# Kernel tuning notes

Measured on AMD Instinct MI355X. Metric: run time of the kernel, lower is better.

Reference implementation:

```python
import jax, jax.numpy as jnp
import numpy as np

B, P, EPG = 1000, 100, 1200  # graphs, nodes/graph, edges/graph
IN, HID, OUT, K = 16, 64, 5, 3


def setup_inputs() -> dict:
    key = jax.random.key(0)
    ks = jax.random.split(key, 12)
    offs = jnp.repeat(jnp.arange(B, dtype=jnp.int32) * P, EPG)
    src = jax.random.randint(ks[0], (B * EPG,), 0, P, dtype=jnp.int32) + offs
    dst = jax.random.randint(ks[1], (B * EPG,), 0, P, dtype=jnp.int32) + offs
    graph_ids = jnp.repeat(jnp.arange(B, dtype=jnp.int32), P)
    feat = jax.random.normal(ks[2], (B * P, IN), dtype=jnp.float32)

    def lin(k1, fan_in, fan_out):
        s = 1.0 / np.sqrt(fan_in)
        return jax.random.uniform(k1, (fan_in, fan_out), jnp.float32, -s, s)

    return {
        'feat': feat, 'src': src, 'dst': dst, 'graph_ids': graph_ids,
        'n_graphs': B,
        'W1': lin(ks[3], K * IN, HID), 'b1': jnp.zeros((HID,), jnp.float32),
        'W2': lin(ks[4], K * HID, HID), 'b2': jnp.zeros((HID,), jnp.float32),
        'W3': lin(ks[5], K * HID, HID), 'b3': jnp.zeros((HID,), jnp.float32),
        'Wfc': lin(ks[6], HID, OUT), 'bfc': jnp.zeros((OUT,), jnp.float32),
    }


def _cheb_conv(x, src, dst, d_invsqrt, W, b, k):
    # DGL ChebConv with lambda_max=2 -> re_norm=1, scaled Laplacian = -D^-1/2 A D^-1/2
    n = x.shape[0]

    def Ax(h):
        msg = (h * d_invsqrt)[src]                      # gather from source nodes
        agg = jax.ops.segment_sum(msg, dst, num_segments=n)
        return agg * d_invsqrt

    Xs = [x]
    if k > 1:
        Xs.append(-Ax(Xs[0]))                           # X1 = L_hat X0
        for _ in range(2, k):
            Xs.append(-2.0 * Ax(Xs[-1]) - Xs[-2])       # X_i = 2 L_hat X_{i-1} - X_{i-2}
    Xt = jnp.concatenate(Xs, axis=1)                    # [n, k*f]
    return Xt @ W + b


def reference(feat, src, dst, graph_ids, n_graphs, W1, b1, W2, b2, W3, b3, Wfc, bfc):
    n = feat.shape[0]
    deg = jax.ops.segment_sum(jnp.ones((src.shape[0],), feat.dtype), dst, num_segments=n)
    d_invsqrt = jnp.where(deg < 1.0, 1.0, deg) ** -0.5
    d_invsqrt = d_invsqrt[:, None]

    h = jax.nn.relu(_cheb_conv(feat, src, dst, d_invsqrt, W1, b1, K))
    h = jax.nn.relu(_cheb_conv(h, src, dst, d_invsqrt, W2, b2, K))
    h = jax.nn.relu(_cheb_conv(h, src, dst, d_invsqrt, W3, b3, K))

    # dgl.mean_nodes: per-graph mean pooling
    counts = jax.ops.segment_sum(jnp.ones((n,), h.dtype), graph_ids, num_segments=n_graphs)
    hg = jax.ops.segment_sum(h, graph_ids, num_segments=n_graphs) / counts[:, None]
    return hg @ Wfc + bfc
```

## Files before the change

kernel.cpp:

```cpp
#include <hip/hip_runtime.h>

#define NGRAPH 1000
#define P      100
#define EPG    1200
#define INF    16
#define HID    64
#define NOUT   5

#define ASTR   88
#define T2OFF  72
#define SLOTA  64
#define SLOTB  80
#define NPAD   112


typedef short short8 __attribute__((ext_vector_type(8)));
typedef float f32x4  __attribute__((ext_vector_type(4)));

__device__ __forceinline__ void bsplit(float x, short& h, short& l) {
    unsigned u = __float_as_uint(x);
    h = (short)(u >> 16);
    float hf = __uint_as_float(u & 0xffff0000u);
    l = (short)(__float_as_uint(x - hf) >> 16);
}

__device__ __forceinline__ void prop_x1(
    float* __restrict__ A, int soff, int dslot,
    const unsigned char* __restrict__ csr_src,
    const int* __restrict__ csr_off,
    const float* __restrict__ dinv, int tid)
{
    const int q4 = (tid & 1) * 4;
    const int n  = tid >> 1;
    if (n < P) {
        const int kb = csr_off[n], ke = csr_off[n + 1];
        float ax = 0.f, ay = 0.f, az = 0.f, aw = 0.f;
        for (int k = kb; k < ke; k++) {
            int s = csr_src[k];
            const float4 x = *(const float4*)&A[s * ASTR + soff + q4];
            ax += x.x; ay += x.y; az += x.z; aw += x.w;
        }
        float dn = dinv[n];
        float m = -dn * dn;
        float4 o; o.x = m * ax; o.y = m * ay; o.z = m * az; o.w = m * aw;
        *(float4*)&A[n * ASTR + dslot + q4] = o;
    }
}

__device__ __forceinline__ void prop_dual(
    float* __restrict__ A, int t1c, int t1n, int ycur, int ynext, bool pre,
    const unsigned char* __restrict__ csr_src,
    const int* __restrict__ csr_off,
    const float* __restrict__ dinv, int tid)
{
    const int q4 = (tid & 1) * 4;
    const int n  = tid >> 1;
    if (n < P) {
        const int kb = csr_off[n], ke = csr_off[n + 1];
        float4 a2 = make_float4(0.f, 0.f, 0.f, 0.f);
        float4 a1 = make_float4(0.f, 0.f, 0.f, 0.f);
        if (pre) {
            for (int k = kb; k < ke; k++) {
                int s = csr_src[k];
                const float* rp = &A[s * ASTR + q4];
                const float4 x2 = *(const float4*)&rp[t1c];
                const float4 x1 = *(const float4*)&rp[ynext];
                a2.x += x2.x; a2.y += x2.y; a2.z += x2.z; a2.w += x2.w;
                a1.x += x1.x; a1.y += x1.y; a1.z += x1.z; a1.w += x1.w;
            }
        } else {
            for (int k = kb; k < ke; k++) {
                int s = csr_src[k];
                const float4 x2 = *(const float4*)&A[s * ASTR + t1c + q4];
                a2.x += x2.x; a2.y += x2.y; a2.z += x2.z; a2.w += x2.w;
            }
        }
        float dn = dinv[n];
        float d2 = dn * dn;
        const float4 y0 = *(const float4*)&A[n * ASTR + ycur + q4];
        float4 o2;
        float m2 = -2.f * d2;
        o2.x = m2 * a2.x - y0.x; o2.y = m2 * a2.y - y0.y;
        o2.z = m2 * a2.z - y0.z; o2.w = m2 * a2.w - y0.w;
        *(float4*)&A[n * ASTR + T2OFF + q4] = o2;
        if (pre) {
            float m1 = -d2;
            float4 o1;
            o1.x = m1 * a1.x; o1.y = m1 * a1.y;
            o1.z = m1 * a1.z; o1.w = m1 * a1.w;
            *(float4*)&A[n * ASTR + t1n + q4] = o1;
        }
    }
}

template <int F, int FINAL>
__device__ __forceinline__ void cheb_layer(
    float* __restrict__ A,
    const unsigned char* __restrict__ csr_src,
    const int* __restrict__ csr_off,
    const float* __restrict__ dinv,
    const float* __restrict__ W, const float* __restrict__ bias,
    int tid)
{
    const int lane = tid & 63;
    const int wv   = tid >> 6;
    const int n16  = lane & 15;
    const int q    = lane >> 4;
    const int ncol = (wv << 4) + n16;
    const float qsc = (q < 3) ? 1.f : 0.f;

    f32x4 acc[7];
#pragma unroll
    for (int t = 0; t < 7; t++) { acc[t][0]=0.f; acc[t][1]=0.f; acc[t][2]=0.f; acc[t][3]=0.f; }

    prop_x1(A, 0, SLOTA, csr_src, csr_off, dinv, tid);
    __syncthreads();

    int t1c = SLOTA, t1n = SLOTB;
    for (int cb = 0; cb < F; cb += 8) {
        const bool pre = (cb + 8 < F);
        prop_dual(A, t1c, t1n, cb, cb + 8, pre, csr_src, csr_off, dinv, tid);
        __syncthreads();

        const int wrow = (q == 0) ? cb : (q == 1) ? (F + cb)
                       : (q == 2) ? (2 * F + cb) : cb;
        short8 bhi, blo;
#pragma unroll
        for (int j = 0; j < 8; j++) {
            float b = W[(wrow + j) * HID + ncol] * qsc;
            short h, l; bsplit(b, h, l);
            bhi[j] = h; blo[j] = l;
        }
        const int aoff = (q == 0) ? cb : (q == 1) ? t1c
                       : (q == 2) ? T2OFF : cb;
#pragma unroll
        for (int t = 0; t < 7; t++) {
            const float* xp = &A[(t * 16 + n16) * ASTR + aoff];
            const float4 v0 = *(const float4*)xp;
            const float4 v1 = *(const float4*)(xp + 4);
            short8 ahi, alo; short h, l;
            bsplit(v0.x * qsc, h, l); ahi[0] = h; alo[0] = l;
            bsplit(v0.y * qsc, h, l); ahi[1] = h; alo[1] = l;
            bsplit(v0.z * qsc, h, l); ahi[2] = h; alo[2] = l;
            bsplit(v0.w * qsc, h, l); ahi[3] = h; alo[3] = l;
            bsplit(v1.x * qsc, h, l); ahi[4] = h; alo[4] = l;
            bsplit(v1.y * qsc, h, l); ahi[5] = h; alo[5] = l;
            bsplit(v1.z * qsc, h, l); ahi[6] = h; alo[6] = l;
            bsplit(v1.w * qsc, h, l); ahi[7] = h; alo[7] = l;
            acc[t] = __builtin_amdgcn_mfma_f32_16x16x32_bf16(ahi, bhi, acc[t], 0, 0, 0);
            acc[t] = __builtin_amdgcn_mfma_f32_16x16x32_bf16(ahi, blo, acc[t], 0, 0, 0);
            acc[t] = __builtin_amdgcn_mfma_f32_16x16x32_bf16(alo, bhi, acc[t], 0, 0, 0);
        }
        __syncthreads();
        int tt = t1c; t1c = t1n; t1n = tt;
    }

    const float bcol = bias[ncol];
    const int rbase = q * 4;
#pragma unroll
    for (int t = 0; t < 7; t++) {
#pragma unroll
        for (int r = 0; r < 4; r++) {
            int row = t * 16 + rbase + r;
            if (row < P) {
                float dn = dinv[row];
                float v = acc[t][r];
                float o;
                if (FINAL) o = fmaxf(v * (1.0f / dn) + bcol, 0.f);
                else       o = fmaxf(v + bcol * dn, 0.f);
                A[row * ASTR + ncol] = o;
            }
        }
    }
    __syncthreads();
}

__global__ __launch_bounds__(256, 4) void gnn_kernel(
    const float* __restrict__ feat,
    const int* __restrict__ src, const int* __restrict__ dst,
    const float* __restrict__ W1, const float* __restrict__ b1,
    const float* __restrict__ W2, const float* __restrict__ b2,
    const float* __restrict__ W3, const float* __restrict__ b3,
    const float* __restrict__ Wfc, const float* __restrict__ bfc,
    float* __restrict__ out)
{
    __shared__ __align__(16) float A[NPAD * ASTR];
    __shared__ unsigned char csr_src[EPG];

    const int g = blockIdx.x;
    const int tid = threadIdx.x;
    const int base = g * P;
    const int* srcg = src + g * EPG;
    const int* dstg = dst + g * EPG;

    int*   deg     = (int*)&A[P * ASTR];
    int*   cur     = (int*)&A[P * ASTR + 100];
    int*   csr_off = (int*)&A[P * ASTR + 200];
    float* dinv    = &A[P * ASTR + 304];
    float* psum    = &A[P * ASTR + 404];

    for (int i = tid; i < P; i += 256) deg[i] = 0;
    __syncthreads();
    for (int e = tid; e < EPG; e += 256) {
        int d = dstg[e] - base;
        atomicAdd(&deg[d], 1);
    }
    __syncthreads();

    for (int i = tid; i < P; i += 256) {
        int dg = deg[i] > 1 ? deg[i] : 1;
        dinv[i] = rsqrtf((float)dg);
    }
    if (tid == 0) {
        int run = 0;
        csr_off[0] = 0;
        for (int i = 0; i < P; i++) { run += deg[i]; csr_off[i + 1] = run; }
    }
    __syncthreads();

    for (int i = tid; i < P * INF / 4; i += 256) {
        int n = i >> 2, fq = (i & 3) * 4;
        float4 v = *(const float4*)&feat[(size_t)base * INF + i * 4];
        float dn = dinv[n];
        v.x *= dn; v.y *= dn; v.z *= dn; v.w *= dn;
        *(float4*)&A[n * ASTR + fq] = v;
    }
    for (int i = tid; i < P; i += 256) cur[i] = csr_off[i];
    __syncthreads();
    for (int e = tid; e < EPG; e += 256) {
        int s = srcg[e] - base;
        int d = dstg[e] - base;
        int pos = atomicAdd(&cur[d], 1);
        csr_src[pos] = (unsigned char)s;
    }
    __syncthreads();

    cheb_layer<INF, 0>(A, csr_src, csr_off, dinv, W1, b1, tid);
    cheb_layer<HID, 0>(A, csr_src, csr_off, dinv, W2, b2, tid);
    cheb_layer<HID, 1>(A, csr_src, csr_off, dinv, W3, b3, tid);

    {
        const int lane = tid & 63, w = tid >> 6;
        float s = 0.f;
        for (int n = w; n < P; n += 4) s += A[n * ASTR + lane];
        psum[w * 64 + lane] = s;
    }
    __syncthreads();
    if (tid < HID) {
        float hg = (psum[tid] + psum[64 + tid] + psum[128 + tid] + psum[192 + tid]) * (1.0f / P);
        psum[256 + tid] = hg;
    }
    __syncthreads();
    if (tid < NOUT) {
        float o = bfc[tid];
        for (int c = 0; c < HID; c++) o += psum[256 + c] * Wfc[c * NOUT + tid];
        out[g * NOUT + tid] = o;
    }
}

extern "C" void kernel_launch(void* const* d_in, const int* in_sizes, int n_in,
                              void* d_out, int out_size, void* d_ws, size_t ws_size,
                              hipStream_t stream)
{
    const float* feat = (const float*)d_in[0];
    const int*   src  = (const int*)d_in[1];
    const int*   dst  = (const int*)d_in[2];
    const float* W1  = (const float*)d_in[5];
    const float* b1  = (const float*)d_in[6];
    const float* W2  = (const float*)d_in[7];
    const float* b2  = (const float*)d_in[8];
    const float* W3  = (const float*)d_in[9];
    const float* b3  = (const float*)d_in[10];
    const float* Wfc = (const float*)d_in[11];
    const float* bfc = (const float*)d_in[12];
    float* out = (float*)d_out;

    gnn_kernel<<<NGRAPH, 256, 0, stream>>>(feat, src, dst,
                                           W1, b1, W2, b2, W3, b3, Wfc, bfc, out);
}
```

Baseline: 191.4 us.

## Pre-split weights into bf16 hi/lo and store activations in packed hi/lo form

```diff
diff --git a/kernel.cpp b/kernel.cpp
--- a/kernel.cpp
+++ b/kernel.cpp
@@ -15,13 +15,51 @@
 
 
 typedef short short8 __attribute__((ext_vector_type(8)));
+typedef int   int4v  __attribute__((ext_vector_type(4)));
 typedef float f32x4  __attribute__((ext_vector_type(4)));
-
-__device__ __forceinline__ void bsplit(float x, short& h, short& l) {
+union HL { int4v i; short8 s; };
+
+__device__ __forceinline__ float funp(float f) {
+    unsigned p = __float_as_uint(f);
+    return __uint_as_float(p & 0xffff0000u) + __uint_as_float(p << 16);
+}
+__device__ __forceinline__ float fpk(float x) {
     unsigned u = __float_as_uint(x);
-    h = (short)(u >> 16);
-    float hf = __uint_as_float(u & 0xffff0000u);
-    l = (short)(__float_as_uint(x - hf) >> 16);
+    unsigned hb = u & 0xffff0000u;
+    float lo = x - __uint_as_float(hb);
+    return __uint_as_float(hb | (__float_as_uint(lo) >> 16));
+}
+
+__global__ __launch_bounds__(256) void wprep(
+    const float* __restrict__ W1, const float* __restrict__ W2,
+    const float* __restrict__ W3, short* __restrict__ wt)
+{
+    const int i0 = blockIdx.x * blockDim.x + threadIdx.x;
+    const int stride = gridDim.x * blockDim.x;
+    for (int e = i0; e < HID * 56; e += stride) {
+        int c = e / 56, r = e % 56;
+        float v = (r < 48) ? W1[r * HID + c] : 0.f;
+        unsigned u = __float_as_uint(v);
+        unsigned hb = u & 0xffff0000u;
+        float lo = v - __uint_as_float(hb);
+        wt[e]        = (short)(hb >> 16);
+        wt[3584 + e] = (short)(__float_as_uint(lo) >> 16);
+    }
+    for (int e = i0; e < HID * 200; e += stride) {
+        int c = e / 200, r = e % 200;
+        float v2 = (r < 192) ? W2[r * HID + c] : 0.f;
+        float v3 = (r < 192) ? W3[r * HID + c] : 0.f;
+        unsigned u2 = __float_as_uint(v2);
+        unsigned h2 = u2 & 0xffff0000u;
+        float l2 = v2 - __uint_as_float(h2);
+        wt[7168 + e]  = (short)(h2 >> 16);
+        wt[19968 + e] = (short)(__float_as_uint(l2) >> 16);
+        unsigned u3 = __float_as_uint(v3);
+        unsigned h3 = u3 & 0xffff0000u;
+        float l3 = v3 - __uint_as_float(h3);
+        wt[32768 + e] = (short)(h3 >> 16);
+        wt[45568 + e] = (short)(__float_as_uint(l3) >> 16);
+    }
 }
 
 __device__ __forceinline__ void prop_x1(
@@ -38,11 +76,12 @@
         for (int k = kb; k < ke; k++) {
             int s = csr_src[k];
             const float4 x = *(const float4*)&A[s * ASTR + soff + q4];
-            ax += x.x; ay += x.y; az += x.z; aw += x.w;
+            ax += funp(x.x); ay += funp(x.y); az += funp(x.z); aw += funp(x.w);
         }
         float dn = dinv[n];
         float m = -dn * dn;
-        float4 o; o.x = m * ax; o.y = m * ay; o.z = m * az; o.w = m * aw;
+        float4 o;
+        o.x = fpk(m * ax); o.y = fpk(m * ay); o.z = fpk(m * az); o.w = fpk(m * aw);
         *(float4*)&A[n * ASTR + dslot + q4] = o;
     }
 }
@@ -65,29 +104,32 @@
                 const float* rp = &A[s * ASTR + q4];
                 const float4 x2 = *(const float4*)&rp[t1c];
                 const float4 x1 = *(const float4*)&rp[ynext];
-                a2.x += x2.x; a2.y += x2.y; a2.z += x2.z; a2.w += x2.w;
-                a1.x += x1.x; a1.y += x1.y; a1.z += x1.z; a1.w += x1.w;
+                a2.x += funp(x2.x); a2.y += funp(x2.y);
+                a2.z += funp(x2.z); a2.w += funp(x2.w);
+                a1.x += funp(x1.x); a1.y += funp(x1.y);
+                a1.z += funp(x1.z); a1.w += funp(x1.w);
             }
         } else {
             for (int k = kb; k < ke; k++) {
                 int s = csr_src[k];
                 const float4 x2 = *(const float4*)&A[s * ASTR + t1c + q4];
-                a2.x += x2.x; a2.y += x2.y; a2.z += x2.z; a2.w += x2.w;
+                a2.x += funp(x2.x); a2.y += funp(x2.y);
+                a2.z += funp(x2.z); a2.w += funp(x2.w);
             }
         }
         float dn = dinv[n];
         float d2 = dn * dn;
         const float4 y0 = *(const float4*)&A[n * ASTR + ycur + q4];
+        float m2 = -2.f * d2;
         float4 o2;
-        float m2 = -2.f * d2;
-        o2.x = m2 * a2.x - y0.x; o2.y = m2 * a2.y - y0.y;
-        o2.z = m2 * a2.z - y0.z; o2.w = m2 * a2.w - y0.w;
+        o2.x = fpk(m2 * a2.x - funp(y0.x)); o2.y = fpk(m2 * a2.y - funp(y0.y));
+        o2.z = fpk(m2 * a2.z - funp(y0.z)); o2.w = fpk(m2 * a2.w - funp(y0.w));
         *(float4*)&A[n * ASTR + T2OFF + q4] = o2;
         if (pre) {
             float m1 = -d2;
             float4 o1;
-            o1.x = m1 * a1.x; o1.y = m1 * a1.y;
-            o1.z = m1 * a1.z; o1.w = m1 * a1.w;
+            o1.x = fpk(m1 * a1.x); o1.y = fpk(m1 * a1.y);
+            o1.z = fpk(m1 * a1.z); o1.w = fpk(m1 * a1.w);
             *(float4*)&A[n * ASTR + t1n + q4] = o1;
         }
     }
@@ -99,15 +141,15 @@
     const unsigned char* __restrict__ csr_src,
     const int* __restrict__ csr_off,
     const float* __restrict__ dinv,
-    const float* __restrict__ W, const float* __restrict__ bias,
-    int tid)
-{
+    const short* __restrict__ whi, const short* __restrict__ wlo,
+    const float* __restrict__ bias, int tid)
+{
+    const int RK   = 3 * F + 8;
     const int lane = tid & 63;
     const int wv   = tid >> 6;
     const int n16  = lane & 15;
     const int q    = lane >> 4;
     const int ncol = (wv << 4) + n16;
-    const float qsc = (q < 3) ? 1.f : 0.f;
 
     f32x4 acc[7];
 #pragma unroll
@@ -122,34 +164,29 @@
         prop_dual(A, t1c, t1n, cb, cb + 8, pre, csr_src, csr_off, dinv, tid);
         __syncthreads();
 
-        const int wrow = (q == 0) ? cb : (q == 1) ? (F + cb)
-                       : (q == 2) ? (2 * F + cb) : cb;
-        short8 bhi, blo;
-#pragma unroll
-        for (int j = 0; j < 8; j++) {
-            float b = W[(wrow + j) * HID + ncol] * qsc;
-            short h, l; bsplit(b, h, l);
-            bhi[j] = h; blo[j] = l;
-        }
+        const int wr = (q == 0) ? cb : (q == 1) ? (F + cb)
+                     : (q == 2) ? (2 * F + cb) : (3 * F);
+        const short8 bhi = *(const short8*)&whi[ncol * RK + wr];
+        const short8 blo = *(const short8*)&wlo[ncol * RK + wr];
+
         const int aoff = (q == 0) ? cb : (q == 1) ? t1c
                        : (q == 2) ? T2OFF : cb;
 #pragma unroll
         for (int t = 0; t < 7; t++) {
-            const float* xp = &A[(t * 16 + n16) * ASTR + aoff];
-            const float4 v0 = *(const float4*)xp;
-            const float4 v1 = *(const float4*)(xp + 4);
-            short8 ahi, alo; short h, l;
-            bsplit(v0.x * qsc, h, l); ahi[0] = h; alo[0] = l;
-            bsplit(v0.y * qsc, h, l); ahi[1] = h; alo[1] = l;
-            bsplit(v0.z * qsc, h, l); ahi[2] = h; alo[2] = l;
-            bsplit(v0.w * qsc, h, l); ahi[3] = h; alo[3] = l;
-            bsplit(v1.x * qsc, h, l); ahi[4] = h; alo[4] = l;
-            bsplit(v1.y * qsc, h, l); ahi[5] = h; alo[5] = l;
-            bsplit(v1.z * qsc, h, l); ahi[6] = h; alo[6] = l;
-            bsplit(v1.w * qsc, h, l); ahi[7] = h; alo[7] = l;
-            acc[t] = __builtin_amdgcn_mfma_f32_16x16x32_bf16(ahi, bhi, acc[t], 0, 0, 0);
-            acc[t] = __builtin_amdgcn_mfma_f32_16x16x32_bf16(ahi, blo, acc[t], 0, 0, 0);
-            acc[t] = __builtin_amdgcn_mfma_f32_16x16x32_bf16(alo, bhi, acc[t], 0, 0, 0);
+            const int4v p0 = *(const int4v*)&A[(t * 16 + n16) * ASTR + aoff];
+            const int4v p1 = *(const int4v*)&A[(t * 16 + n16) * ASTR + aoff + 4];
+            HL hi, lo;
+            hi.i[0] = (int)((((unsigned)p0[0]) >> 16) | (((unsigned)p0[1]) & 0xffff0000u));
+            hi.i[1] = (int)((((unsigned)p0[2]) >> 16) | (((unsigned)p0[3]) & 0xffff0000u));
+            hi.i[2] = (int)((((unsigned)p1[0]) >> 16) | (((unsigned)p1[1]) & 0xffff0000u));
+            hi.i[3] = (int)((((unsigned)p1[2]) >> 16) | (((unsigned)p1[3]) & 0xffff0000u));
+            lo.i[0] = (int)((p0[0] & 0xffff) | (((unsigned)p0[1]) << 16));
+            lo.i[1] = (int)((p0[2] & 0xffff) | (((unsigned)p0[3]) << 16));
+            lo.i[2] = (int)((p1[0] & 0xffff) | (((unsigned)p1[1]) << 16));
+            lo.i[3] = (int)((p1[2] & 0xffff) | (((unsigned)p1[3]) << 16));
+            acc[t] = __builtin_amdgcn_mfma_f32_16x16x32_bf16(hi.s, bhi, acc[t], 0, 0, 0);
+            acc[t] = __builtin_amdgcn_mfma_f32_16x16x32_bf16(hi.s, blo, acc[t], 0, 0, 0);
+            acc[t] = __builtin_amdgcn_mfma_f32_16x16x32_bf16(lo.s, bhi, acc[t], 0, 0, 0);
         }
         __syncthreads();
         int tt = t1c; t1c = t1n; t1n = tt;
@@ -167,7 +204,7 @@
                 float v = acc[t][r];
                 float o;
                 if (FINAL) o = fmaxf(v * (1.0f / dn) + bcol, 0.f);
-                else       o = fmaxf(v + bcol * dn, 0.f);
+                else       o = fpk(fmaxf(v + bcol * dn, 0.f));
                 A[row * ASTR + ncol] = o;
             }
         }
@@ -178,10 +215,10 @@
 __global__ __launch_bounds__(256, 4) void gnn_kernel(
     const float* __restrict__ feat,
     const int* __restrict__ src, const int* __restrict__ dst,
-    const float* __restrict__ W1, const float* __restrict__ b1,
-    const float* __restrict__ W2, const float* __restrict__ b2,
-    const float* __restrict__ W3, const float* __restrict__ b3,
+    const float* __restrict__ b1, const float* __restrict__ b2,
+    const float* __restrict__ b3,
     const float* __restrict__ Wfc, const float* __restrict__ bfc,
+    const short* __restrict__ wt,
     float* __restrict__ out)
 {
     __shared__ __align__(16) float A[NPAD * ASTR];
@@ -222,8 +259,10 @@
         int n = i >> 2, fq = (i & 3) * 4;
         float4 v = *(const float4*)&feat[(size_t)base * INF + i * 4];
         float dn = dinv[n];
-        v.x *= dn; v.y *= dn; v.z *= dn; v.w *= dn;
-        *(float4*)&A[n * ASTR + fq] = v;
+        float4 o;
+        o.x = fpk(v.x * dn); o.y = fpk(v.y * dn);
+        o.z = fpk(v.z * dn); o.w = fpk(v.w * dn);
+        *(float4*)&A[n * ASTR + fq] = o;
     }
     for (int i = tid; i < P; i += 256) cur[i] = csr_off[i];
     __syncthreads();
@@ -235,9 +274,9 @@
     }
     __syncthreads();
 
-    cheb_layer<INF, 0>(A, csr_src, csr_off, dinv, W1, b1, tid);
-    cheb_layer<HID, 0>(A, csr_src, csr_off, dinv, W2, b2, tid);
-    cheb_layer<HID, 1>(A, csr_src, csr_off, dinv, W3, b3, tid);
+    cheb_layer<INF, 0>(A, csr_src, csr_off, dinv, wt,         wt + 3584,  b1, tid);
+    cheb_layer<HID, 0>(A, csr_src, csr_off, dinv, wt + 7168,  wt + 19968, b2, tid);
+    cheb_layer<HID, 1>(A, csr_src, csr_off, dinv, wt + 32768, wt + 45568, b3, tid);
 
     {
         const int lane = tid & 63, w = tid >> 6;
@@ -274,7 +313,9 @@
     const float* Wfc = (const float*)d_in[11];
     const float* bfc = (const float*)d_in[12];
     float* out = (float*)d_out;
-
+    short* wt = (short*)d_ws;
+
+    wprep<<<64, 256, 0, stream>>>(W1, W2, W3, wt);
     gnn_kernel<<<NGRAPH, 256, 0, stream>>>(feat, src, dst,
-                                           W1, b1, W2, b2, W3, b3, Wfc, bfc, out);
-}
+                                           b1, b2, b3, Wfc, bfc, wt, out);
+}
```

Result: slower. 235.3 us (+22.9%).
